# Optimization experiments

Hardware: AMD Instinct MI355X
Metric: run time of the kernel (lower is better)

Reference implementation:

```python
import jax, jax.numpy as jnp
import numpy as np

N_POINTS = 10000
N_EVENTS = 1_000_000


def setup_inputs() -> dict:
    key = jax.random.key(0)
    k1, k2, k3 = jax.random.split(key, 3)
    # data columns: [node_i, node_j, time_point]; stored as float, cast to int in forward
    data = jax.random.randint(k1, (N_EVENTS, 3), 0, N_POINTS).astype(jnp.float32)
    beta = jax.random.normal(k2, (1, 1), dtype=jnp.float32)
    z0 = jax.random.uniform(k3, (N_POINTS, 2), dtype=jnp.float32) * 0.5
    return {"data": data, "t0": 0, "tn": 0, "beta": beta, "z0": z0}


def reference(data, t0, tn, beta, z0):
    i = data[:, 0].astype(jnp.int32)
    j = data[:, 1].astype(jnp.int32)
    # full pairwise squared euclidean distance matrix [N, N]
    sq = jnp.sum(z0 * z0, axis=1)  # [N]
    dist = sq[:, None] + sq[None, :] - 2.0 * (z0 @ z0.T)  # [N, N]
    d_ij = dist[i, j]  # gather sparse subset [E]
    log_intensities = beta[0, 0] - d_ij
    event_intensity = jnp.sum(log_intensities)
    non_event_intensity = jnp.sum(jnp.exp(log_intensities))
    log_likelihood = event_intensity - non_event_intensity
    return -log_likelihood
```

## Files before the change

kernel.cpp:

```cpp
#include <hip/hip_runtime.h>

#define BLOCK 256
#define VPT   4

__global__ __launch_bounds__(BLOCK) void nd_partial_kernel(
    const float* __restrict__ data,
    const float* __restrict__ beta,
    const float* __restrict__ z0,
    float* __restrict__ partials,
    int E)
{
    const float b = beta[0];
    const float4* __restrict__ d4 = (const float4*)data;
    const float2* __restrict__ z2 = (const float2*)z0;

    float s_log = 0.0f;
    float s_exp = 0.0f;

    int t  = blockIdx.x * BLOCK + threadIdx.x;
    int e0 = t * VPT;

    if (e0 + VPT <= E) {
        float4 va = d4[3 * t + 0];
        float4 vb = d4[3 * t + 1];
        float4 vc = d4[3 * t + 2];
        int i0 = (int)va.x, j0 = (int)va.y;
        int i1 = (int)va.w, j1 = (int)vb.x;
        int i2 = (int)vb.z, j2 = (int)vb.w;
        int i3 = (int)vc.y, j3 = (int)vc.z;

        float2 pi0 = z2[i0], pj0 = z2[j0];
        float2 pi1 = z2[i1], pj1 = z2[j1];
        float2 pi2 = z2[i2], pj2 = z2[j2];
        float2 pi3 = z2[i3], pj3 = z2[j3];

        float dx0 = pi0.x - pj0.x, dy0 = pi0.y - pj0.y;
        float dx1 = pi1.x - pj1.x, dy1 = pi1.y - pj1.y;
        float dx2 = pi2.x - pj2.x, dy2 = pi2.y - pj2.y;
        float dx3 = pi3.x - pj3.x, dy3 = pi3.y - pj3.y;

        float l0 = b - (dx0 * dx0 + dy0 * dy0);
        float l1 = b - (dx1 * dx1 + dy1 * dy1);
        float l2 = b - (dx2 * dx2 + dy2 * dy2);
        float l3 = b - (dx3 * dx3 + dy3 * dy3);

        s_log = (l0 + l1) + (l2 + l3);
        s_exp = (__expf(l0) + __expf(l1)) + (__expf(l2) + __expf(l3));
    } else {
        for (int e = e0; e < E; ++e) {
            int i = (int)data[3 * e + 0];
            int j = (int)data[3 * e + 1];
            float2 pi = z2[i], pj = z2[j];
            float dx = pi.x - pj.x, dy = pi.y - pj.y;
            float li = b - (dx * dx + dy * dy);
            s_log += li;
            s_exp += __expf(li);
        }
    }

    for (int off = 32; off > 0; off >>= 1) {
        s_log += __shfl_down(s_log, off, 64);
        s_exp += __shfl_down(s_exp, off, 64);
    }

    __shared__ float lds1[BLOCK / 64];
    __shared__ float lds2[BLOCK / 64];
    int lane = threadIdx.x & 63;
    int wave = threadIdx.x >> 6;
    if (lane == 0) { lds1[wave] = s_log; lds2[wave] = s_exp; }
    __syncthreads();
    if (threadIdx.x == 0) {
        float t1 = 0.0f, t2 = 0.0f;
        #pragma unroll
        for (int w = 0; w < BLOCK / 64; ++w) { t1 += lds1[w]; t2 += lds2[w]; }
        partials[2 * blockIdx.x + 0] = t1;
        partials[2 * blockIdx.x + 1] = t2;
    }
}

__global__ __launch_bounds__(256) void nd_final_kernel(
    const float* __restrict__ partials,
    float* __restrict__ out,
    int nblk)
{
    float s1 = 0.0f, s2 = 0.0f;
    for (int idx = threadIdx.x; idx < nblk; idx += 256) {
        s1 += partials[2 * idx + 0];
        s2 += partials[2 * idx + 1];
    }
    for (int off = 32; off > 0; off >>= 1) {
        s1 += __shfl_down(s1, off, 64);
        s2 += __shfl_down(s2, off, 64);
    }
    __shared__ float lds1[4];
    __shared__ float lds2[4];
    int lane = threadIdx.x & 63;
    int wave = threadIdx.x >> 6;
    if (lane == 0) { lds1[wave] = s1; lds2[wave] = s2; }
    __syncthreads();
    if (threadIdx.x == 0) {
        float t1 = 0.0f, t2 = 0.0f;
        #pragma unroll
        for (int w = 0; w < 4; ++w) { t1 += lds1[w]; t2 += lds2[w]; }
        out[0] = t2 - t1;
    }
}

extern "C" void kernel_launch(void* const* d_in, const int* in_sizes, int n_in,
                              void* d_out, int out_size, void* d_ws, size_t ws_size,
                              hipStream_t stream) {
    const float* data = (const float*)d_in[0];
    const float* beta = (const float*)d_in[3];
    const float* z0   = (const float*)d_in[4];
    float* out        = (float*)d_out;
    float* partials   = (float*)d_ws;

    int E = in_sizes[0] / 3;
    int threads = (E + VPT - 1) / VPT;
    int nblk = (threads + BLOCK - 1) / BLOCK;

    nd_partial_kernel<<<nblk, BLOCK, 0, stream>>>(data, beta, z0, partials, E);
    nd_final_kernel<<<1, 256, 0, stream>>>(partials, out, nblk);
}
```

Measured before the change: 74.75 us.

## Stage most of z0 in LDS per block, with nontemporal event loads

```diff
diff --git a/kernel.cpp b/kernel.cpp
--- a/kernel.cpp
+++ b/kernel.cpp
@@ -1,7 +1,10 @@
 #include <hip/hip_runtime.h>
 
-#define BLOCK 256
+#define BLOCK 512
 #define VPT   4
+#define ZS    8064
+
+typedef float fx4 __attribute__((ext_vector_type(4)));
 
 __global__ __launch_bounds__(BLOCK) void nd_partial_kernel(
     const float* __restrict__ data,
@@ -10,9 +13,21 @@
     float* __restrict__ partials,
     int E)
 {
+    __shared__ __align__(16) float2 zs[ZS];
+    __shared__ float lds1[BLOCK / 64];
+    __shared__ float lds2[BLOCK / 64];
+
+    const float2* __restrict__ z2 = (const float2*)z0;
+
+    {
+        const float4* __restrict__ z4 = (const float4*)z0;
+        float4* zs4 = (float4*)zs;
+        for (int k = threadIdx.x; k < ZS / 2; k += BLOCK) zs4[k] = z4[k];
+    }
+    __syncthreads();
+
     const float b = beta[0];
-    const float4* __restrict__ d4 = (const float4*)data;
-    const float2* __restrict__ z2 = (const float2*)z0;
+    const fx4* __restrict__ d4 = (const fx4*)data;
 
     float s_log = 0.0f;
     float s_exp = 0.0f;
@@ -21,18 +36,22 @@
     int e0 = t * VPT;
 
     if (e0 + VPT <= E) {
-        float4 va = d4[3 * t + 0];
-        float4 vb = d4[3 * t + 1];
-        float4 vc = d4[3 * t + 2];
+        fx4 va = __builtin_nontemporal_load(&d4[3 * t + 0]);
+        fx4 vb = __builtin_nontemporal_load(&d4[3 * t + 1]);
+        fx4 vc = __builtin_nontemporal_load(&d4[3 * t + 2]);
         int i0 = (int)va.x, j0 = (int)va.y;
         int i1 = (int)va.w, j1 = (int)vb.x;
         int i2 = (int)vb.z, j2 = (int)vb.w;
         int i3 = (int)vc.y, j3 = (int)vc.z;
 
-        float2 pi0 = z2[i0], pj0 = z2[j0];
-        float2 pi1 = z2[i1], pj1 = z2[j1];
-        float2 pi2 = z2[i2], pj2 = z2[j2];
-        float2 pi3 = z2[i3], pj3 = z2[j3];
+        float2 pi0 = (i0 < ZS) ? zs[i0] : z2[i0];
+        float2 pj0 = (j0 < ZS) ? zs[j0] : z2[j0];
+        float2 pi1 = (i1 < ZS) ? zs[i1] : z2[i1];
+        float2 pj1 = (j1 < ZS) ? zs[j1] : z2[j1];
+        float2 pi2 = (i2 < ZS) ? zs[i2] : z2[i2];
+        float2 pj2 = (j2 < ZS) ? zs[j2] : z2[j2];
+        float2 pi3 = (i3 < ZS) ? zs[i3] : z2[i3];
+        float2 pj3 = (j3 < ZS) ? zs[j3] : z2[j3];
 
         float dx0 = pi0.x - pj0.x, dy0 = pi0.y - pj0.y;
         float dx1 = pi1.x - pj1.x, dy1 = pi1.y - pj1.y;
@@ -50,7 +69,8 @@
         for (int e = e0; e < E; ++e) {
             int i = (int)data[3 * e + 0];
             int j = (int)data[3 * e + 1];
-            float2 pi = z2[i], pj = z2[j];
+            float2 pi = (i < ZS) ? zs[i] : z2[i];
+            float2 pj = (j < ZS) ? zs[j] : z2[j];
             float dx = pi.x - pj.x, dy = pi.y - pj.y;
             float li = b - (dx * dx + dy * dy);
             s_log += li;
@@ -63,8 +83,6 @@
         s_exp += __shfl_down(s_exp, off, 64);
     }
 
-    __shared__ float lds1[BLOCK / 64];
-    __shared__ float lds2[BLOCK / 64];
     int lane = threadIdx.x & 63;
     int wave = threadIdx.x >> 6;
     if (lane == 0) { lds1[wave] = s_log; lds2[wave] = s_exp; }
```

After: 73.04 us. -2.3%, faster.
